# Performance work log

Hardware: AMD Instinct MI355X
Metric: run time of the kernel (lower is better)

Reference implementation:

```python
import jax, jax.numpy as jnp
import numpy as np

B, N, D_IN, D_OUT = 16, 4096, 256, 128


def setup_inputs() -> dict:
    key = jax.random.key(0)
    ks = jax.random.split(key, 7)
    s_proj = float(np.sqrt(2.0 / D_IN))   # kaiming-ish scale
    s_mlp = float(np.sqrt(2.0 / D_OUT))
    return {
        "X": jax.random.normal(ks[0], (B, N, D_IN), dtype=jnp.float32),
        "W_proj": jax.random.normal(ks[1], (D_IN, D_OUT), dtype=jnp.float32) * s_proj,
        "b_proj": jnp.zeros((D_OUT,), dtype=jnp.float32),
        "W1": jax.random.normal(ks[2], (D_OUT, D_OUT), dtype=jnp.float32) * s_mlp,
        "b1": jnp.zeros((D_OUT,), dtype=jnp.float32),
        "W2": jax.random.normal(ks[3], (D_OUT, D_OUT), dtype=jnp.float32) * s_mlp,
        "b2": jnp.zeros((D_OUT,), dtype=jnp.float32),
    }


def reference(X, W_proj, b_proj, W1, b1, W2, b2):
    # proj: Linear(input_dim, output_dim)
    X = jnp.einsum("bnd,de->bne", X, W_proj) + b_proj
    # mlp: FeedForwardNetwork(D,D,D, num_layers=2) == Linear -> ReLU -> Linear
    X = jax.nn.relu(jnp.einsum("bnd,de->bne", X, W1) + b1)
    X = jnp.einsum("bnd,de->bne", X, W2) + b2
    # leave-one-out sum over the N axis: for each row i, sum of all rows j != i.
    # Identical math to the masked (B,N,N,D) expand-reduce in the torch source.
    return X.sum(axis=1, keepdims=True) - X
```

## Files before the change

kernel.cpp:

```cpp
#include <hip/hip_runtime.h>
#include <stdint.h>

#define D_IN  256
#define D_OUT 128
#define NSEQ  4096
#define NB    16
#define TILE_M 64
#define GRID_M ((NB * NSEQ) / TILE_M)
#define LDS_BYTES 16384

typedef __bf16 bf16x8 __attribute__((ext_vector_type(8)));
typedef float  f32x4  __attribute__((ext_vector_type(4)));

__device__ __forceinline__ unsigned short f2bf(float f) {
  union { float f; unsigned int u; } a; a.f = f;
  unsigned int r = a.u + 0x7FFFu + ((a.u >> 16) & 1u);
  return (unsigned short)(r >> 16);
}
__device__ __forceinline__ float bf2f(unsigned short u) {
  union { unsigned int u; float f; } a; a.u = ((unsigned int)u) << 16;
  return a.f;
}

__global__ __launch_bounds__(256) void prep_weights(
    const float* __restrict__ Wp, const float* __restrict__ W1, const float* __restrict__ W2,
    unsigned short* __restrict__ WpT, unsigned short* __restrict__ W1T, unsigned short* __restrict__ W2T) {
  int t = blockIdx.x * 256 + threadIdx.x;
  if (t < 256 * 128) {
    int k = t >> 7, n = t & 127;
    WpT[n * 256 + k] = f2bf(Wp[t]);
  } else if (t < 256 * 128 + 128 * 128) {
    int t2 = t - 256 * 128; int k = t2 >> 7, n = t2 & 127;
    W1T[n * 128 + k] = f2bf(W1[t2]);
  } else {
    int t3 = t - 256 * 128 - 128 * 128; int k = t3 >> 7, n = t3 & 127;
    W2T[n * 128 + k] = f2bf(W2[t3]);
  }
}

template <bool USE_WS>
__global__ __launch_bounds__(256, 3) void fused3(
    const float* __restrict__ X,
    const unsigned short* __restrict__ WpT,
    const unsigned short* __restrict__ W1T,
    const unsigned short* __restrict__ W2T,
    const float* __restrict__ bproj, const float* __restrict__ b1v, const float* __restrict__ b2v,
    unsigned short* __restrict__ Y3, float* __restrict__ out, float* __restrict__ P) {
  extern __shared__ char smem[];
  unsigned short* buf0 = (unsigned short*)smem;

  const int tid  = threadIdx.x;
  const int lane = tid & 63;
  const int w    = tid >> 6;
  const int q    = lane >> 4;
  const int l16  = lane & 15;
  const int rowbase = blockIdx.x * TILE_M;

  const int col0 = w * 32 + l16;
  const int col1 = col0 + 16;

  f32x4 acc[4][2];
  bf16x8 bA[8], bB[8];

#pragma unroll
  for (int ks = 0; ks < 4; ++ks) {
    bA[ks * 2 + 0] = *(const bf16x8*)(WpT + (size_t)col0 * 256 + ks * 32 + q * 8);
    bA[ks * 2 + 1] = *(const bf16x8*)(WpT + (size_t)col1 * 256 + ks * 32 + q * 8);
  }

#pragma unroll
  for (int it = 0; it < 8; ++it) {
    int i = tid + it * 256;
    int r = i >> 5, c4 = (i & 31) << 2;
    const float4 v = *(const float4*)(X + (size_t)(rowbase + r) * D_IN + c4);
    ushort4 u; u.x = f2bf(v.x); u.y = f2bf(v.y); u.z = f2bf(v.z); u.w = f2bf(v.w);
    *(ushort4*)(buf0 + r * 128 + ((((c4 >> 3) ^ (r & 15)) << 3) + (c4 & 7))) = u;
  }

#pragma unroll
  for (int rt = 0; rt < 4; ++rt)
#pragma unroll
    for (int ct = 0; ct < 2; ++ct) acc[rt][ct] = (f32x4){0.f, 0.f, 0.f, 0.f};

  __syncthreads();

#pragma unroll
  for (int ks = 0; ks < 4; ++ks) {
    bB[ks * 2 + 0] = *(const bf16x8*)(WpT + (size_t)col0 * 256 + 128 + ks * 32 + q * 8);
    bB[ks * 2 + 1] = *(const bf16x8*)(WpT + (size_t)col1 * 256 + 128 + ks * 32 + q * 8);
  }

#pragma unroll
  for (int ks = 0; ks < 4; ++ks) {
#pragma unroll
    for (int rt = 0; rt < 4; ++rt) {
      bf16x8 a = *(const bf16x8*)(buf0 + (rt * 16 + l16) * 128 + (((4 * ks + q) ^ l16) << 3));
      acc[rt][0] = __builtin_amdgcn_mfma_f32_16x16x32_bf16(a, bA[ks * 2 + 0], acc[rt][0], 0, 0, 0);
      acc[rt][1] = __builtin_amdgcn_mfma_f32_16x16x32_bf16(a, bA[ks * 2 + 1], acc[rt][1], 0, 0, 0);
    }
  }
  __syncthreads();

#pragma unroll
  for (int it = 0; it < 8; ++it) {
    int i = tid + it * 256;
    int r = i >> 5, c4 = (i & 31) << 2;
    const float4 v = *(const float4*)(X + (size_t)(rowbase + r) * D_IN + 128 + c4);
    ushort4 u; u.x = f2bf(v.x); u.y = f2bf(v.y); u.z = f2bf(v.z); u.w = f2bf(v.w);
    *(ushort4*)(buf0 + r * 128 + ((((c4 >> 3) ^ (r & 15)) << 3) + (c4 & 7))) = u;
  }
  __syncthreads();

#pragma unroll
  for (int ks = 0; ks < 4; ++ks) {
    bA[ks * 2 + 0] = *(const bf16x8*)(W1T + (size_t)col0 * 128 + ks * 32 + q * 8);
    bA[ks * 2 + 1] = *(const bf16x8*)(W1T + (size_t)col1 * 128 + ks * 32 + q * 8);
  }

#pragma unroll
  for (int ks = 0; ks < 4; ++ks) {
#pragma unroll
    for (int rt = 0; rt < 4; ++rt) {
      bf16x8 a = *(const bf16x8*)(buf0 + (rt * 16 + l16) * 128 + (((4 * ks + q) ^ l16) << 3));
      acc[rt][0] = __builtin_amdgcn_mfma_f32_16x16x32_bf16(a, bB[ks * 2 + 0], acc[rt][0], 0, 0, 0);
      acc[rt][1] = __builtin_amdgcn_mfma_f32_16x16x32_bf16(a, bB[ks * 2 + 1], acc[rt][1], 0, 0, 0);
    }
  }
  __syncthreads();

  {
    const float bp0 = bproj[col0], bp1 = bproj[col1];
#pragma unroll
    for (int rt = 0; rt < 4; ++rt)
#pragma unroll
      for (int r = 0; r < 4; ++r) {
        int row = rt * 16 + q * 4 + r;
        int sw = (row & 15) << 3;
        buf0[row * 128 + ((((col0 >> 3) << 3) ^ sw) + (col0 & 7))] = f2bf(acc[rt][0][r] + bp0);
        buf0[row * 128 + ((((col1 >> 3) << 3) ^ sw) + (col1 & 7))] = f2bf(acc[rt][1][r] + bp1);
      }
  }
  __syncthreads();

#pragma unroll
  for (int ks = 0; ks < 4; ++ks) {
    bB[ks * 2 + 0] = *(const bf16x8*)(W2T + (size_t)col0 * 128 + ks * 32 + q * 8);
    bB[ks * 2 + 1] = *(const bf16x8*)(W2T + (size_t)col1 * 128 + ks * 32 + q * 8);
  }

#pragma unroll
  for (int rt = 0; rt < 4; ++rt)
#pragma unroll
    for (int ct = 0; ct < 2; ++ct) acc[rt][ct] = (f32x4){0.f, 0.f, 0.f, 0.f};
#pragma unroll
  for (int ks = 0; ks < 4; ++ks) {
#pragma unroll
    for (int rt = 0; rt < 4; ++rt) {
      bf16x8 a = *(const bf16x8*)(buf0 + (rt * 16 + l16) * 128 + (((4 * ks + q) ^ l16) << 3));
      acc[rt][0] = __builtin_amdgcn_mfma_f32_16x16x32_bf16(a, bA[ks * 2 + 0], acc[rt][0], 0, 0, 0);
      acc[rt][1] = __builtin_amdgcn_mfma_f32_16x16x32_bf16(a, bA[ks * 2 + 1], acc[rt][1], 0, 0, 0);
    }
  }
  __syncthreads();

  {
    const float bb0 = b1v[col0], bb1 = b1v[col1];
#pragma unroll
    for (int rt = 0; rt < 4; ++rt)
#pragma unroll
      for (int r = 0; r < 4; ++r) {
        int row = rt * 16 + q * 4 + r;
        int sw = (row & 15) << 3;
        float v0 = acc[rt][0][r] + bb0; v0 = v0 > 0.f ? v0 : 0.f;
        float v1 = acc[rt][1][r] + bb1; v1 = v1 > 0.f ? v1 : 0.f;
        buf0[row * 128 + ((((col0 >> 3) << 3) ^ sw) + (col0 & 7))] = f2bf(v0);
        buf0[row * 128 + ((((col1 >> 3) << 3) ^ sw) + (col1 & 7))] = f2bf(v1);
      }
  }
  __syncthreads();

#pragma unroll
  for (int rt = 0; rt < 4; ++rt)
#pragma unroll
    for (int ct = 0; ct < 2; ++ct) acc[rt][ct] = (f32x4){0.f, 0.f, 0.f, 0.f};
#pragma unroll
  for (int ks = 0; ks < 4; ++ks) {
#pragma unroll
    for (int rt = 0; rt < 4; ++rt) {
      bf16x8 a = *(const bf16x8*)(buf0 + (rt * 16 + l16) * 128 + (((4 * ks + q) ^ l16) << 3));
      acc[rt][0] = __builtin_amdgcn_mfma_f32_16x16x32_bf16(a, bB[ks * 2 + 0], acc[rt][0], 0, 0, 0);
      acc[rt][1] = __builtin_amdgcn_mfma_f32_16x16x32_bf16(a, bB[ks * 2 + 1], acc[rt][1], 0, 0, 0);
    }
  }
  __syncthreads();

  {
    const float bb0 = b2v[col0], bb1 = b2v[col1];
    float s0 = 0.f, s1 = 0.f;
#pragma unroll
    for (int rt = 0; rt < 4; ++rt)
#pragma unroll
      for (int r = 0; r < 4; ++r) {
        int row = rt * 16 + q * 4 + r;
        int sw = (row & 15) << 3;
        float v0 = acc[rt][0][r] + bb0;
        float v1 = acc[rt][1][r] + bb1;
        s0 += v0; s1 += v1;
        buf0[row * 128 + ((((col0 >> 3) << 3) ^ sw) + (col0 & 7))] = f2bf(v0);
        buf0[row * 128 + ((((col1 >> 3) << 3) ^ sw) + (col1 & 7))] = f2bf(v1);
      }
    s0 += __shfl_down(s0, 16); s0 += __shfl_down(s0, 32);
    s1 += __shfl_down(s1, 16); s1 += __shfl_down(s1, 32);
    if (lane < 16) {
      P[(size_t)blockIdx.x * 128 + col0] = s0;
      P[(size_t)blockIdx.x * 128 + col1] = s1;
    }
  }
  __syncthreads();

  if (USE_WS) {
#pragma unroll
    for (int it = 0; it < 4; ++it) {
      int i = tid + it * 256;
      int r = i >> 4, g = i & 15;
      *(uint4*)(Y3 + (size_t)(rowbase + r) * 128 + g * 8) =
          *(const uint4*)(buf0 + r * 128 + ((g ^ (r & 15)) << 3));
    }
  } else {
#pragma unroll
    for (int it = 0; it < 8; ++it) {
      int i = tid + it * 256;
      int r = i >> 5, c4 = (i & 31) << 2;
      ushort4 u = *(const ushort4*)(buf0 + r * 128 + ((((c4 >> 3) ^ (r & 15)) << 3) + (c4 & 7)));
      float4 v; v.x = bf2f(u.x); v.y = bf2f(u.y); v.z = bf2f(u.z); v.w = bf2f(u.w);
      *(float4*)(out + (size_t)(rowbase + r) * D_OUT + c4) = v;
    }
  }
}

__global__ __launch_bounds__(256) void reduce_S(const float* __restrict__ P, float* __restrict__ S) {
  __shared__ float tmp[128];
  int b = blockIdx.x;
  int col = threadIdx.x & 127;
  int h = threadIdx.x >> 7;
  float s = 0.f;
#pragma unroll
  for (int i = 0; i < 32; ++i) s += P[(size_t)(b * 64 + h * 32 + i) * 128 + col];
  if (h == 1) tmp[col] = s;
  __syncthreads();
  if (h == 0) S[b * 128 + col] = s + tmp[col];
}

__global__ __launch_bounds__(256) void finalize_ws(
    float* __restrict__ out, const unsigned short* __restrict__ Y3, const float* __restrict__ S) {
  size_t g = (size_t)blockIdx.x * 256 + threadIdx.x;
  size_t base = g * 8;
  int row = (int)(base >> 7);
  int col = (int)(base & 127);
  int b = row >> 12;
  uint4 u = *(const uint4*)(Y3 + base);
  float4 s0 = *(const float4*)(S + (b << 7) + col);
  float4 s1 = *(const float4*)(S + (b << 7) + col + 4);
  union { unsigned int u; float f; } t;
  float4 o0, o1;
  t.u = u.x << 16;          o0.x = s0.x - t.f;
  t.u = u.x & 0xFFFF0000u;  o0.y = s0.y - t.f;
  t.u = u.y << 16;          o0.z = s0.z - t.f;
  t.u = u.y & 0xFFFF0000u;  o0.w = s0.w - t.f;
  t.u = u.z << 16;          o1.x = s1.x - t.f;
  t.u = u.z & 0xFFFF0000u;  o1.y = s1.y - t.f;
  t.u = u.w << 16;          o1.z = s1.z - t.f;
  t.u = u.w & 0xFFFF0000u;  o1.w = s1.w - t.f;
  *(float4*)(out + base) = o0;
  *(float4*)(out + base + 4) = o1;
}

__global__ __launch_bounds__(256) void finalize_ip(float* __restrict__ out, const float* __restrict__ S) {
  size_t g = (size_t)blockIdx.x * 256 + threadIdx.x;
  size_t base = g * 8;
  int row = (int)(base >> 7);
  int col = (int)(base & 127);
  int b = row >> 12;
  float4 s0 = *(const float4*)(S + (b << 7) + col);
  float4 s1 = *(const float4*)(S + (b << 7) + col + 4);
  float4 y0 = *(const float4*)(out + base);
  float4 y1 = *(const float4*)(out + base + 4);
  float4 o0, o1;
  o0.x = s0.x - y0.x; o0.y = s0.y - y0.y; o0.z = s0.z - y0.z; o0.w = s0.w - y0.w;
  o1.x = s1.x - y1.x; o1.y = s1.y - y1.y; o1.z = s1.z - y1.z; o1.w = s1.w - y1.w;
  *(float4*)(out + base) = o0;
  *(float4*)(out + base + 4) = o1;
}

extern "C" void kernel_launch(void* const* d_in, const int* in_sizes, int n_in,
                              void* d_out, int out_size, void* d_ws, size_t ws_size,
                              hipStream_t stream) {
  const float* X  = (const float*)d_in[0];
  const float* Wp = (const float*)d_in[1];
  const float* bp = (const float*)d_in[2];
  const float* W1 = (const float*)d_in[3];
  const float* b1 = (const float*)d_in[4];
  const float* W2 = (const float*)d_in[5];
  const float* b2 = (const float*)d_in[6];
  float* out = (float*)d_out;

  char* ws = (char*)d_ws;
  float* S = (float*)ws;
  unsigned short* WpT = (unsigned short*)(ws + 8192);
  unsigned short* W1T = (unsigned short*)(ws + 8192 + 65536);
  unsigned short* W2T = (unsigned short*)(ws + 8192 + 65536 + 32768);
  float* P = (float*)(ws + 8192 + 131072);
  unsigned short* Y3 = (unsigned short*)(ws + 8192 + 131072 + 524288);

  const size_t need = 8192 + 131072 + 524288 + (size_t)NB * NSEQ * D_OUT * 2;
  const bool use_ws = ws_size >= need;

  prep_weights<<<256, 256, 0, stream>>>(Wp, W1, W2, WpT, W1T, W2T);

  const int fin_blocks = (NB * NSEQ * D_OUT) / (8 * 256);
  if (use_ws) {
    fused3<true><<<GRID_M, 256, LDS_BYTES, stream>>>(X, WpT, W1T, W2T, bp, b1, b2, Y3, out, P);
    reduce_S<<<NB, 256, 0, stream>>>(P, S);
    finalize_ws<<<fin_blocks, 256, 0, stream>>>(out, Y3, S);
  } else {
    fused3<false><<<GRID_M, 256, LDS_BYTES, stream>>>(X, WpT, W1T, W2T, bp, b1, b2, Y3, out, P);
    reduce_S<<<NB, 256, 0, stream>>>(P, S);
    finalize_ip<<<fin_blocks, 256, 0, stream>>>(out, S);
  }
}
```

Baseline: 138.4 us.

## Double-buffer LDS, preload all weights, overlap second X half load with GEMM

Splits LDS into two 16KB buffers so the second half of X can be loaded into registers during the first K-half MFMA pass, then written to the other buffer. Alternating buffers between stages removes several __syncthreads. All weight fragments are loaded into registers up front. f2bf now uses the native __bf16 conversion. The cost is more registers and LDS, so occupancy drops from 3 to 2 blocks per CU.

```diff
diff --git a/kernel.cpp b/kernel.cpp
--- a/kernel.cpp
+++ b/kernel.cpp
@@ -7,15 +7,15 @@
 #define NB    16
 #define TILE_M 64
 #define GRID_M ((NB * NSEQ) / TILE_M)
-#define LDS_BYTES 16384
+#define LDS_BYTES 32768
 
 typedef __bf16 bf16x8 __attribute__((ext_vector_type(8)));
 typedef float  f32x4  __attribute__((ext_vector_type(4)));
 
 __device__ __forceinline__ unsigned short f2bf(float f) {
-  union { float f; unsigned int u; } a; a.f = f;
-  unsigned int r = a.u + 0x7FFFu + ((a.u >> 16) & 1u);
-  return (unsigned short)(r >> 16);
+  __bf16 h = (__bf16)f;
+  union { __bf16 h; unsigned short u; } c; c.h = h;
+  return c.u;
 }
 __device__ __forceinline__ float bf2f(unsigned short u) {
   union { unsigned int u; float f; } a; a.u = ((unsigned int)u) << 16;
@@ -39,15 +39,16 @@
 }
 
 template <bool USE_WS>
-__global__ __launch_bounds__(256, 3) void fused3(
+__global__ __launch_bounds__(256, 2) void fused3(
     const float* __restrict__ X,
     const unsigned short* __restrict__ WpT,
     const unsigned short* __restrict__ W1T,
     const unsigned short* __restrict__ W2T,
     const float* __restrict__ bproj, const float* __restrict__ b1v, const float* __restrict__ b2v,
     unsigned short* __restrict__ Y3, float* __restrict__ out, float* __restrict__ P) {
-  extern __shared__ char smem[];
-  unsigned short* buf0 = (unsigned short*)smem;
+  extern __shared__ unsigned short smem[];
+  unsigned short* bufA = smem;
+  unsigned short* bufB = smem + 8192;
 
   const int tid  = threadIdx.x;
   const int lane = tid & 63;
@@ -55,18 +56,22 @@
   const int q    = lane >> 4;
   const int l16  = lane & 15;
   const int rowbase = blockIdx.x * TILE_M;
-
   const int col0 = w * 32 + l16;
   const int col1 = col0 + 16;
 
-  f32x4 acc[4][2];
-  bf16x8 bA[8], bB[8];
-
+  bf16x8 wp0[2][4], wp1[2][4], w1f[2][4], w2f[2][4];
 #pragma unroll
   for (int ks = 0; ks < 4; ++ks) {
-    bA[ks * 2 + 0] = *(const bf16x8*)(WpT + (size_t)col0 * 256 + ks * 32 + q * 8);
-    bA[ks * 2 + 1] = *(const bf16x8*)(WpT + (size_t)col1 * 256 + ks * 32 + q * 8);
-  }
+    wp0[0][ks] = *(const bf16x8*)(WpT + (size_t)col0 * 256 + ks * 32 + q * 8);
+    wp0[1][ks] = *(const bf16x8*)(WpT + (size_t)col1 * 256 + ks * 32 + q * 8);
+    wp1[0][ks] = *(const bf16x8*)(WpT + (size_t)col0 * 256 + 128 + ks * 32 + q * 8);
+    wp1[1][ks] = *(const bf16x8*)(WpT + (size_t)col1 * 256 + 128 + ks * 32 + q * 8);
+    w1f[0][ks] = *(const bf16x8*)(W1T + (size_t)col0 * 128 + ks * 32 + q * 8);
+    w1f[1][ks] = *(const bf16x8*)(W1T + (size_t)col1 * 128 + ks * 32 + q * 8);
+    w2f[0][ks] = *(const bf16x8*)(W2T + (size_t)col0 * 128 + ks * 32 + q * 8);
+    w2f[1][ks] = *(const bf16x8*)(W2T + (size_t)col1 * 128 + ks * 32 + q * 8);
+  }
+  __builtin_amdgcn_sched_barrier(0);
 
 #pragma unroll
   for (int it = 0; it < 8; ++it) {
@@ -74,59 +79,51 @@
     int r = i >> 5, c4 = (i & 31) << 2;
     const float4 v = *(const float4*)(X + (size_t)(rowbase + r) * D_IN + c4);
     ushort4 u; u.x = f2bf(v.x); u.y = f2bf(v.y); u.z = f2bf(v.z); u.w = f2bf(v.w);
-    *(ushort4*)(buf0 + r * 128 + ((((c4 >> 3) ^ (r & 15)) << 3) + (c4 & 7))) = u;
-  }
-
-#pragma unroll
-  for (int rt = 0; rt < 4; ++rt)
-#pragma unroll
-    for (int ct = 0; ct < 2; ++ct) acc[rt][ct] = (f32x4){0.f, 0.f, 0.f, 0.f};
-
-  __syncthreads();
-
-#pragma unroll
-  for (int ks = 0; ks < 4; ++ks) {
-    bB[ks * 2 + 0] = *(const bf16x8*)(WpT + (size_t)col0 * 256 + 128 + ks * 32 + q * 8);
-    bB[ks * 2 + 1] = *(const bf16x8*)(WpT + (size_t)col1 * 256 + 128 + ks * 32 + q * 8);
-  }
-
-#pragma unroll
-  for (int ks = 0; ks < 4; ++ks) {
-#pragma unroll
-    for (int rt = 0; rt < 4; ++rt) {
-      bf16x8 a = *(const bf16x8*)(buf0 + (rt * 16 + l16) * 128 + (((4 * ks + q) ^ l16) << 3));
-      acc[rt][0] = __builtin_amdgcn_mfma_f32_16x16x32_bf16(a, bA[ks * 2 + 0], acc[rt][0], 0, 0, 0);
-      acc[rt][1] = __builtin_amdgcn_mfma_f32_16x16x32_bf16(a, bA[ks * 2 + 1], acc[rt][1], 0, 0, 0);
-    }
-  }
-  __syncthreads();
-
+    *(ushort4*)(bufA + r * 128 + ((((c4 >> 3) ^ (r & 15)) << 3) + (c4 & 7))) = u;
+  }
+
+  f32x4 acc[4][2];
+#pragma unroll
+  for (int rt = 0; rt < 4; ++rt) {
+    acc[rt][0] = (f32x4){0.f, 0.f, 0.f, 0.f};
+    acc[rt][1] = (f32x4){0.f, 0.f, 0.f, 0.f};
+  }
+  __syncthreads();
+
+  float4 xv[8];
 #pragma unroll
   for (int it = 0; it < 8; ++it) {
     int i = tid + it * 256;
     int r = i >> 5, c4 = (i & 31) << 2;
-    const float4 v = *(const float4*)(X + (size_t)(rowbase + r) * D_IN + 128 + c4);
-    ushort4 u; u.x = f2bf(v.x); u.y = f2bf(v.y); u.z = f2bf(v.z); u.w = f2bf(v.w);
-    *(ushort4*)(buf0 + r * 128 + ((((c4 >> 3) ^ (r & 15)) << 3) + (c4 & 7))) = u;
-  }
-  __syncthreads();
-
-#pragma unroll
-  for (int ks = 0; ks < 4; ++ks) {
-    bA[ks * 2 + 0] = *(const bf16x8*)(W1T + (size_t)col0 * 128 + ks * 32 + q * 8);
-    bA[ks * 2 + 1] = *(const bf16x8*)(W1T + (size_t)col1 * 128 + ks * 32 + q * 8);
-  }
-
-#pragma unroll
-  for (int ks = 0; ks < 4; ++ks) {
+    xv[it] = *(const float4*)(X + (size_t)(rowbase + r) * D_IN + 128 + c4);
+  }
+
+#pragma unroll
+  for (int ks = 0; ks < 4; ++ks)
 #pragma unroll
     for (int rt = 0; rt < 4; ++rt) {
-      bf16x8 a = *(const bf16x8*)(buf0 + (rt * 16 + l16) * 128 + (((4 * ks + q) ^ l16) << 3));
-      acc[rt][0] = __builtin_amdgcn_mfma_f32_16x16x32_bf16(a, bB[ks * 2 + 0], acc[rt][0], 0, 0, 0);
-      acc[rt][1] = __builtin_amdgcn_mfma_f32_16x16x32_bf16(a, bB[ks * 2 + 1], acc[rt][1], 0, 0, 0);
-    }
-  }
-  __syncthreads();
+      bf16x8 a = *(const bf16x8*)(bufA + (rt * 16 + l16) * 128 + (((4 * ks + q) ^ l16) << 3));
+      acc[rt][0] = __builtin_amdgcn_mfma_f32_16x16x32_bf16(a, wp0[0][ks], acc[rt][0], 0, 0, 0);
+      acc[rt][1] = __builtin_amdgcn_mfma_f32_16x16x32_bf16(a, wp0[1][ks], acc[rt][1], 0, 0, 0);
+    }
+
+#pragma unroll
+  for (int it = 0; it < 8; ++it) {
+    int i = tid + it * 256;
+    int r = i >> 5, c4 = (i & 31) << 2;
+    ushort4 u; u.x = f2bf(xv[it].x); u.y = f2bf(xv[it].y); u.z = f2bf(xv[it].z); u.w = f2bf(xv[it].w);
+    *(ushort4*)(bufB + r * 128 + ((((c4 >> 3) ^ (r & 15)) << 3) + (c4 & 7))) = u;
+  }
+  __syncthreads();
+
+#pragma unroll
+  for (int ks = 0; ks < 4; ++ks)
+#pragma unroll
+    for (int rt = 0; rt < 4; ++rt) {
+      bf16x8 a = *(const bf16x8*)(bufB + (rt * 16 + l16) * 128 + (((4 * ks + q) ^ l16) << 3));
+      acc[rt][0] = __builtin_amdgcn_mfma_f32_16x16x32_bf16(a, wp1[0][ks], acc[rt][0], 0, 0, 0);
+      acc[rt][1] = __builtin_amdgcn_mfma_f32_16x16x32_bf16(a, wp1[1][ks], acc[rt][1], 0, 0, 0);
+    }
 
   {
     const float bp0 = bproj[col0], bp1 = bproj[col1];
@@ -136,32 +133,25 @@
       for (int r = 0; r < 4; ++r) {
         int row = rt * 16 + q * 4 + r;
         int sw = (row & 15) << 3;
-        buf0[row * 128 + ((((col0 >> 3) << 3) ^ sw) + (col0 & 7))] = f2bf(acc[rt][0][r] + bp0);
-        buf0[row * 128 + ((((col1 >> 3) << 3) ^ sw) + (col1 & 7))] = f2bf(acc[rt][1][r] + bp1);
+        bufA[row * 128 + ((((col0 >> 3) << 3) ^ sw) + (col0 & 7))] = f2bf(acc[rt][0][r] + bp0);
+        bufA[row * 128 + ((((col1 >> 3) << 3) ^ sw) + (col1 & 7))] = f2bf(acc[rt][1][r] + bp1);
       }
   }
   __syncthreads();
 
 #pragma unroll
-  for (int ks = 0; ks < 4; ++ks) {
-    bB[ks * 2 + 0] = *(const bf16x8*)(W2T + (size_t)col0 * 128 + ks * 32 + q * 8);
-    bB[ks * 2 + 1] = *(const bf16x8*)(W2T + (size_t)col1 * 128 + ks * 32 + q * 8);
-  }
-
-#pragma unroll
-  for (int rt = 0; rt < 4; ++rt)
-#pragma unroll
-    for (int ct = 0; ct < 2; ++ct) acc[rt][ct] = (f32x4){0.f, 0.f, 0.f, 0.f};
-#pragma unroll
-  for (int ks = 0; ks < 4; ++ks) {
+  for (int rt = 0; rt < 4; ++rt) {
+    acc[rt][0] = (f32x4){0.f, 0.f, 0.f, 0.f};
+    acc[rt][1] = (f32x4){0.f, 0.f, 0.f, 0.f};
+  }
+#pragma unroll
+  for (int ks = 0; ks < 4; ++ks)
 #pragma unroll
     for (int rt = 0; rt < 4; ++rt) {
-      bf16x8 a = *(const bf16x8*)(buf0 + (rt * 16 + l16) * 128 + (((4 * ks + q) ^ l16) << 3));
-      acc[rt][0] = __builtin_amdgcn_mfma_f32_16x16x32_bf16(a, bA[ks * 2 + 0], acc[rt][0], 0, 0, 0);
-      acc[rt][1] = __builtin_amdgcn_mfma_f32_16x16x32_bf16(a, bA[ks * 2 + 1], acc[rt][1], 0, 0, 0);
-    }
-  }
-  __syncthreads();
+      bf16x8 a = *(const bf16x8*)(bufA + (rt * 16 + l16) * 128 + (((4 * ks + q) ^ l16) << 3));
+      acc[rt][0] = __builtin_amdgcn_mfma_f32_16x16x32_bf16(a, w1f[0][ks], acc[rt][0], 0, 0, 0);
+      acc[rt][1] = __builtin_amdgcn_mfma_f32_16x16x32_bf16(a, w1f[1][ks], acc[rt][1], 0, 0, 0);
+    }
 
   {
     const float bb0 = b1v[col0], bb1 = b1v[col1];
@@ -173,26 +163,25 @@
         int sw = (row & 15) << 3;
         float v0 = acc[rt][0][r] + bb0; v0 = v0 > 0.f ? v0 : 0.f;
         float v1 = acc[rt][1][r] + bb1; v1 = v1 > 0.f ? v1 : 0.f;
-        buf0[row * 128 + ((((col0 >> 3) << 3) ^ sw) + (col0 & 7))] = f2bf(v0);
-        buf0[row * 128 + ((((col1 >> 3) << 3) ^ sw) + (col1 & 7))] = f2bf(v1);
+        bufB[row * 128 + ((((col0 >> 3) << 3) ^ sw) + (col0 & 7))] = f2bf(v0);
+        bufB[row * 128 + ((((col1 >> 3) << 3) ^ sw) + (col1 & 7))] = f2bf(v1);
       }
   }
   __syncthreads();
 
 #pragma unroll
-  for (int rt = 0; rt < 4; ++rt)
-#pragma unroll
-    for (int ct = 0; ct < 2; ++ct) acc[rt][ct] = (f32x4){0.f, 0.f, 0.f, 0.f};
-#pragma unroll
-  for (int ks = 0; ks < 4; ++ks) {
+  for (int rt = 0; rt < 4; ++rt) {
+    acc[rt][0] = (f32x4){0.f, 0.f, 0.f, 0.f};
+    acc[rt][1] = (f32x4){0.f, 0.f, 0.f, 0.f};
+  }
+#pragma unroll
+  for (int ks = 0; ks < 4; ++ks)
 #pragma unroll
     for (int rt = 0; rt < 4; ++rt) {
-      bf16x8 a = *(const bf16x8*)(buf0 + (rt * 16 + l16) * 128 + (((4 * ks + q) ^ l16) << 3));
-      acc[rt][0] = __builtin_amdgcn_mfma_f32_16x16x32_bf16(a, bB[ks * 2 + 0], acc[rt][0], 0, 0, 0);
-      acc[rt][1] = __builtin_amdgcn_mfma_f32_16x16x32_bf16(a, bB[ks * 2 + 1], acc[rt][1], 0, 0, 0);
-    }
-  }
-  __syncthreads();
+      bf16x8 a = *(const bf16x8*)(bufB + (rt * 16 + l16) * 128 + (((4 * ks + q) ^ l16) << 3));
+      acc[rt][0] = __builtin_amdgcn_mfma_f32_16x16x32_bf16(a, w2f[0][ks], acc[rt][0], 0, 0, 0);
+      acc[rt][1] = __builtin_amdgcn_mfma_f32_16x16x32_bf16(a, w2f[1][ks], acc[rt][1], 0, 0, 0);
+    }
 
   {
     const float bb0 = b2v[col0], bb1 = b2v[col1];
@@ -206,8 +195,8 @@
         float v0 = acc[rt][0][r] + bb0;
         float v1 = acc[rt][1][r] + bb1;
         s0 += v0; s1 += v1;
-        buf0[row * 128 + ((((col0 >> 3) << 3) ^ sw) + (col0 & 7))] = f2bf(v0);
-        buf0[row * 128 + ((((col1 >> 3) << 3) ^ sw) + (col1 & 7))] = f2bf(v1);
+        bufA[row * 128 + ((((col0 >> 3) << 3) ^ sw) + (col0 & 7))] = f2bf(v0);
+        bufA[row * 128 + ((((col1 >> 3) << 3) ^ sw) + (col1 & 7))] = f2bf(v1);
       }
     s0 += __shfl_down(s0, 16); s0 += __shfl_down(s0, 32);
     s1 += __shfl_down(s1, 16); s1 += __shfl_down(s1, 32);
@@ -224,14 +213,14 @@
       int i = tid + it * 256;
       int r = i >> 4, g = i & 15;
       *(uint4*)(Y3 + (size_t)(rowbase + r) * 128 + g * 8) =
-          *(const uint4*)(buf0 + r * 128 + ((g ^ (r & 15)) << 3));
+          *(const uint4*)(bufA + r * 128 + ((g ^ (r & 15)) << 3));
     }
   } else {
 #pragma unroll
     for (int it = 0; it < 8; ++it) {
       int i = tid + it * 256;
       int r = i >> 5, c4 = (i & 31) << 2;
-      ushort4 u = *(const ushort4*)(buf0 + r * 128 + ((((c4 >> 3) ^ (r & 15)) << 3) + (c4 & 7)));
+      ushort4 u = *(const ushort4*)(bufA + r * 128 + ((((c4 >> 3) ^ (r & 15)) << 3) + (c4 & 7)));
       float4 v; v.x = bf2f(u.x); v.y = bf2f(u.y); v.z = bf2f(u.z); v.w = bf2f(u.w);
       *(float4*)(out + (size_t)(rowbase + r) * D_OUT + c4) = v;
     }
@@ -261,16 +250,16 @@
   uint4 u = *(const uint4*)(Y3 + base);
   float4 s0 = *(const float4*)(S + (b << 7) + col);
   float4 s1 = *(const float4*)(S + (b << 7) + col + 4);
-  union { unsigned int u; float f; } t;
+  union { unsigned int uu; float f; } t;
   float4 o0, o1;
-  t.u = u.x << 16;          o0.x = s0.x - t.f;
-  t.u = u.x & 0xFFFF0000u;  o0.y = s0.y - t.f;
-  t.u = u.y << 16;          o0.z = s0.z - t.f;
-  t.u = u.y & 0xFFFF0000u;  o0.w = s0.w - t.f;
-  t.u = u.z << 16;          o1.x = s1.x - t.f;
-  t.u = u.z & 0xFFFF0000u;  o1.y = s1.y - t.f;
-  t.u = u.w << 16;          o1.z = s1.z - t.f;
-  t.u = u.w & 0xFFFF0000u;  o1.w = s1.w - t.f;
+  t.uu = u.x << 16;          o0.x = s0.x - t.f;
+  t.uu = u.x & 0xFFFF0000u;  o0.y = s0.y - t.f;
+  t.uu = u.y << 16;          o0.z = s0.z - t.f;
+  t.uu = u.y & 0xFFFF0000u;  o0.w = s0.w - t.f;
+  t.uu = u.z << 16;          o1.x = s1.x - t.f;
+  t.uu = u.z & 0xFFFF0000u;  o1.y = s1.y - t.f;
+  t.uu = u.w << 16;          o1.z = s1.z - t.f;
+  t.uu = u.w & 0xFFFF0000u;  o1.w = s1.w - t.f;
   *(float4*)(out + base) = o0;
   *(float4*)(out + base + 4) = o1;
 }
```

Measured after the change: 137.2 us. Within noise of the previous version (-0.9%).
